# Kernel tuning notes

Measured on AMD Instinct MI355X. Metric: run time of the kernel, lower is better.

## Reference

```python
import jax, jax.numpy as jnp
import numpy as np

# geomloss SamplesLoss('sinkhorn', blur=0.5, scaling=0.9, reach=None) defaults: p=2, debias=True
P = 2
BLUR = 0.5
SCALING = 0.9


def _sqdist_half(a, b):
    # C(x,y) = |x-y|^2 / 2  (geomloss p=2 cost), shape [N, M]
    a2 = jnp.sum(a * a, axis=1)
    b2 = jnp.sum(b * b, axis=1)
    return 0.5 * (a2[:, None] + b2[None, :]) - a @ b.T


def _softmin(eps, C, h):
    # softmin_tensorized: -eps * logsumexp_j( h_j - C_ij / eps ),  h = log-weights + dual/eps
    return -eps * jax.nn.logsumexp(h[None, :] - C / eps, axis=1)


def _eps_schedule(x, y):
    # geomloss epsilon_schedule: anneal eps from diameter^p down to blur^p by scaling^p
    xn, yn = np.asarray(x), np.asarray(y)
    mins = np.minimum(xn.min(axis=0), yn.min(axis=0))
    maxs = np.maximum(xn.max(axis=0), yn.max(axis=0))
    diameter = float(np.linalg.norm(maxs - mins))
    eps_list = [diameter ** P]
    eps_list += [float(np.exp(e)) for e in
                 np.arange(P * np.log(diameter), P * np.log(BLUR), P * np.log(SCALING))]
    eps_list += [BLUR ** P]
    return eps_list


def _sinkhorn_divergence(x, y, eps_list):
    N, M = x.shape[0], y.shape[0]
    C_xy = _sqdist_half(x, y)
    C_yx = C_xy.T
    C_xx = _sqdist_half(x, x)
    C_yy = _sqdist_half(y, y)
    a_log = jnp.full((N,), -float(np.log(N)), dtype=x.dtype)  # uniform weights, log domain
    b_log = jnp.full((M,), -float(np.log(M)), dtype=x.dtype)

    sg = jax.lax.stop_gradient
    Cxy_d, Cyx_d = sg(C_xy), sg(C_yx)
    Cxx_d, Cyy_d = sg(C_xx), sg(C_yy)

    # init at largest eps (= diameter^p)
    eps0 = eps_list[0]
    f_ba = _softmin(eps0, Cxy_d, b_log)
    g_ab = _softmin(eps0, Cyx_d, a_log)
    f_aa = _softmin(eps0, Cxx_d, a_log)
    g_bb = _softmin(eps0, Cyy_d, b_log)

    # symmetric (averaged) Sinkhorn updates along the eps-scaling schedule (no grad, like geomloss)
    for eps in eps_list:
        ft_ba = _softmin(eps, Cxy_d, b_log + g_ab / eps)
        gt_ab = _softmin(eps, Cyx_d, a_log + f_ba / eps)
        ft_aa = _softmin(eps, Cxx_d, a_log + f_aa / eps)
        gt_bb = _softmin(eps, Cyy_d, b_log + g_bb / eps)
        f_ba, g_ab = 0.5 * (f_ba + ft_ba), 0.5 * (g_ab + gt_ab)
        f_aa, g_bb = 0.5 * (f_aa + ft_aa), 0.5 * (g_bb + gt_bb)

    # last extrapolation at eps = blur^p; gradient flows only through the cost matrices here
    eps = eps_list[-1]
    f_ba, g_ab = (_softmin(eps, C_xy, sg(b_log + g_ab / eps)),
                  _softmin(eps, C_yx, sg(a_log + f_ba / eps)))
    f_aa = _softmin(eps, C_xx, sg(a_log + f_aa / eps))
    g_bb = _softmin(eps, C_yy, sg(b_log + g_bb / eps))

    # debiased divergence: <alpha, f_ba - f_aa> + <beta, g_ab - g_bb> (uniform weights -> mean)
    return jnp.mean(f_ba - f_aa) + jnp.mean(g_ab - g_bb)


def setup_inputs() -> dict:
    key = jax.random.key(0)
    kx, ky = jax.random.split(key)
    x = jax.random.normal(kx, (4096, 32), dtype=jnp.float32)
    y = jax.random.normal(ky, (4096, 32), dtype=jnp.float32)
    return {"x": x, "y": y}


def reference(x, y):
    eps_list = _eps_schedule(x, y)  # data-dependent schedule computed eagerly (as geomloss does)
    return _sinkhorn_divergence(x, y, eps_list)
```

## Files before the change

### kernel.cpp

```cpp
#include <hip/hip_runtime.h>
#include <math.h>

#define NPTS 4096
#define DIM  32
#define MAXSLOTS 50
#define NTHREADS 256
#define ITHREADS 512
#define NELEM 131072

#define WS_N2X   0
#define WS_N2Y   4096
#define WS_PMIN  8192
#define WS_PMAX  10240
#define WS_EPS   12288
#define WS_MODE  12352
#define WS_DUAL  12416
#define DUALSZ   16384
#define WS_BF    45184

#define M_SKIP   0
#define M_INIT   1
#define M_AVG    2
#define M_ASSIGN 3

typedef short    short8 __attribute__((ext_vector_type(8)));
typedef _Float16 half8  __attribute__((ext_vector_type(8)));
typedef float    f32x4  __attribute__((ext_vector_type(4)));

__device__ __forceinline__ float exp2fast(float a){
#if __has_builtin(__builtin_amdgcn_exp2f)
    return __builtin_amdgcn_exp2f(a);
#else
    return exp2f(a);
#endif
}
__device__ __forceinline__ float log2fast(float a){
#if __has_builtin(__builtin_amdgcn_logf)
    return __builtin_amdgcn_logf(a);
#else
    return log2f(a);
#endif
}

__device__ __forceinline__ short8 pack8(const float* src){
    float4 v0 = ((const float4*)src)[0];
    float4 v1 = ((const float4*)src)[1];
    float vs[8] = {v0.x, v0.y, v0.z, v0.w, v1.x, v1.y, v1.z, v1.w};
    short hv[8];
#pragma unroll
    for (int i = 0; i < 8; i++) {
        union { _Float16 f; short s; } u;
        u.f = (_Float16)vs[i];
        hv[i] = u.s;
    }
    short8 r = {hv[0],hv[1],hv[2],hv[3],hv[4],hv[5],hv[6],hv[7]};
    return r;
}

__global__ void sink_setup(const float* __restrict__ x, const float* __restrict__ y,
                           float* __restrict__ ws, unsigned short* __restrict__ bf)
{
    __shared__ float2 mm[8][32];
    const int t = threadIdx.x;
    const int b = blockIdx.x;
    const int gtid = b * 256 + t;

    {
        int e = gtid * 8;
        *(short8*)((short*)bf + e)         = pack8(x + e);
        *(short8*)((short*)bf + NELEM + e) = pack8(y + e);
    }
    if (gtid < 2 * NPTS) {
        const float* src = (gtid < NPTS) ? (x + (size_t)gtid * DIM)
                                         : (y + (size_t)(gtid - NPTS) * DIM);
        const float4* s4 = (const float4*)src;
        float acc = 0.f;
#pragma unroll
        for (int q = 0; q < 8; q++) {
            float4 v = s4[q];
            acc += v.x*v.x + v.y*v.y + v.z*v.z + v.w*v.w;
        }
        ws[gtid] = 0.5f * acc;
    }
    {
        int d = t & 31, rg = t >> 5;
        float mn = 3.4e38f, mx = -3.4e38f;
#pragma unroll
        for (int k = 0; k < 16; k++) {
            int row = b * 128 + k * 8 + rg;
            const float* src = (row < NPTS) ? (x + (size_t)row * DIM)
                                            : (y + (size_t)(row - NPTS) * DIM);
            float v = src[d];
            mn = fminf(mn, v); mx = fmaxf(mx, v);
        }
        mm[rg][d] = make_float2(mn, mx);
    }
    __syncthreads();
    if (t < 32) {
        float2 a = mm[0][t];
#pragma unroll
        for (int g = 1; g < 8; g++) {
            float2 p = mm[g][t];
            a.x = fminf(a.x, p.x); a.y = fmaxf(a.y, p.y);
        }
        ws[WS_PMIN + b * 32 + t] = a.x;
        ws[WS_PMAX + b * 32 + t] = a.y;
    }
}

__global__ void sink_sched(float* __restrict__ ws)
{
    __shared__ float mins[32], maxs[32];
    int t = threadIdx.x;
    if (t < 32) {
        float mn = 3.4e38f, mx = -3.4e38f;
        for (int b = 0; b < 64; b++) {
            mn = fminf(mn, ws[WS_PMIN + b * 32 + t]);
            mx = fmaxf(mx, ws[WS_PMAX + b * 32 + t]);
        }
        mins[t] = mn; maxs[t] = mx;
    }
    __syncthreads();
    if (t == 0) {
        float dia2 = 0.f;
        for (int d = 0; d < 32; d++) {
            float df = maxs[d] - mins[d];
            dia2 += df * df;
        }
        float dia = sqrtf(dia2);
        float* eps = ws + WS_EPS;
        int*  mode = (int*)(ws + WS_MODE);
        double ld    = log((double)dia);
        double start = 2.0 * ld;
        double stop  = 2.0 * log(0.5);
        double step  = 2.0 * log(0.9);
        int K = (int)ceil((stop - start) / step);
        if (K < 0) K = 0;
        if (K > MAXSLOTS - 4) K = MAXSLOTS - 4;
        eps[0] = dia * dia; mode[0] = M_INIT;
        eps[1] = dia * dia; mode[1] = M_AVG;
        for (int k = 0; k < K; k++) {
            eps[2 + k] = (float)exp(start + step * (double)k);
            mode[2 + k] = M_AVG;
        }
        eps[2 + K] = 0.25f; mode[2 + K] = M_AVG;
        eps[3 + K] = 0.25f; mode[3 + K] = M_ASSIGN;
        for (int s = 4 + K; s < MAXSLOTS; s++) { eps[s] = 0.25f; mode[s] = M_SKIP; }
        mode[62] = K + 4;
    }
}

#define GLSE(T, R, G) \
    { float v0 = fmaf(ca##T[0][R], ie2, hpq[(G)*4 + 0]); \
      float v1 = fmaf(ca##T[1][R], ie2, hpq[(G)*4 + 1]); \
      float v2 = fmaf(ca##T[2][R], ie2, hpq[(G)*4 + 2]); \
      float v3 = fmaf(ca##T[3][R], ie2, hpq[(G)*4 + 3]); \
      float gm = fmaxf(fmaxf(v0, v1), v2); \
      float nm = fmaxf(fmaxf(gm, v3), ms##T[R]); \
      float er = exp2fast(ms##T[R] - nm); \
      float e0 = exp2fast(v0 - nm); \
      float e1 = exp2fast(v1 - nm); \
      float e2 = exp2fast(v2 - nm); \
      float e3 = exp2fast(v3 - nm); \
      ss##T[R] = fmaf(ss##T[R], er, (e0 + e1) + (e2 + e3)); \
      ms##T[R] = nm; }

__global__ __launch_bounds__(ITHREADS, 4) void sink_iter(float* __restrict__ ws, int slot)
{
    const int t = threadIdx.x;
    const int mode = ((const int*)(ws + WS_MODE))[slot];
    if (mode == M_SKIP) return;

    const float eps     = ws[WS_EPS + slot];
    const float inv_eps = 1.0f / eps;
    const float L2E     = 1.4426950408889634f;
    const float LN2     = 0.6931471805599453f;
    const float ie2     = inv_eps * L2E;
    const float hbase   = -8.317766166719343f;
    const float don     = (mode == M_INIT) ? 0.0f : 1.0f;

    const int bm   = blockIdx.x >> 7;
    const int tile = blockIdx.x & 127;
    const int S    = (blockIdx.x * 5) & 31;
    const int rowIsX = (bm == 0 || bm == 2);
    const int colIsX = (bm == 1 || bm == 2);

    const short* bf = (const short*)(ws + WS_BF);
    const short* rbase = bf + (rowIsX ? 0 : NELEM);
    const short* cbase = bf + (colIsX ? 0 : NELEM);
    const float* rn2 = ws + (rowIsX ? WS_N2X : WS_N2Y);
    const float* cn2 = ws + (colIsX ? WS_N2X : WS_N2Y);

    const float* bufold = ws + WS_DUAL + (slot & 1) * DUALSZ;
    float*       bufnew = ws + WS_DUAL + ((slot + 1) & 1) * DUALSZ;
    const int dualsel = (bm == 0) ? 1 : (bm == 1) ? 0 : bm;
    const float* dual   = bufold + dualsel * NPTS;
    const float* oldout = bufold + bm * NPTS;
    float*       out    = bufnew + bm * NPTS;

    __shared__ float2 parts[8][32];

    const int lane = t & 63;
    const int wv   = t >> 6;
    const int lr   = lane & 15;
    const int lk   = (lane >> 4) * 8;

    const int ar0 = tile * 32 + lr;
    const half8 a0 = *(const half8*)(rbase + ar0 * DIM + lk);
    const half8 a1 = *(const half8*)(rbase + (ar0 + 16) * DIM + lk);

    const int colbase = wv * 512;
    const short* cwb = cbase + (size_t)colbase * DIM;
    const int laneoff = lr * DIM + lk;

    float hpq[32];
#pragma unroll
    for (int p = 0; p < 32; p++) {
        const int j = colbase + ((p + S) & 31) * 16 + lr;
        hpq[p] = (hbase + fmaf(don, dual[j], -cn2[j]) * inv_eps) * L2E;
    }

    half8 bh[4];
#pragma unroll
    for (int p = 0; p < 4; p++) {
        const int w = (p + S) & 31;
        bh[p] = *(const half8*)(cwb + w * (16 * DIM) + laneoff);
    }

    float ms0[4] = {-INFINITY, -INFINITY, -INFINITY, -INFINITY};
    float ms1[4] = {-INFINITY, -INFINITY, -INFINITY, -INFINITY};
    float ss0[4] = {0.f, 0.f, 0.f, 0.f};
    float ss1[4] = {0.f, 0.f, 0.f, 0.f};
    f32x4 ca0[4], ca1[4];

#pragma unroll
    for (int g = 0; g < 8; g++) {
#pragma unroll
        for (int sl = 0; sl < 4; sl++) {
            const int ct = g * 4 + sl;
            const half8 hB = bh[sl];
            f32x4 u0 = {0.f, 0.f, 0.f, 0.f};
            f32x4 u1 = {0.f, 0.f, 0.f, 0.f};
            u0 = __builtin_amdgcn_mfma_f32_16x16x32_f16(a0, hB, u0, 0, 0, 0);
            u1 = __builtin_amdgcn_mfma_f32_16x16x32_f16(a1, hB, u1, 0, 0, 0);
            if (ct < 28) {
                const int w = ((ct + 4) + S) & 31;
                bh[sl] = *(const half8*)(cwb + w * (16 * DIM) + laneoff);
            }
            ca0[sl] = u0;
            ca1[sl] = u1;
        }
        GLSE(0, 0, g) GLSE(0, 1, g) GLSE(0, 2, g) GLSE(0, 3, g)
        GLSE(1, 0, g) GLSE(1, 1, g) GLSE(1, 2, g) GLSE(1, 3, g)
    }

#pragma unroll
    for (int wm = 1; wm <= 8; wm <<= 1) {
#pragma unroll
        for (int r = 0; r < 4; r++) {
            float om, os, nm;
            om = __shfl_xor(ms0[r], wm, 64); os = __shfl_xor(ss0[r], wm, 64);
            nm = fmaxf(ms0[r], om);
            ss0[r] = fmaf(ss0[r], exp2fast(ms0[r] - nm), os * exp2fast(om - nm));
            ms0[r] = nm;
            om = __shfl_xor(ms1[r], wm, 64); os = __shfl_xor(ss1[r], wm, 64);
            nm = fmaxf(ms1[r], om);
            ss1[r] = fmaf(ss1[r], exp2fast(ms1[r] - nm), os * exp2fast(om - nm));
            ms1[r] = nm;
        }
    }
    if (lr == 0) {
        const int g4 = (lane >> 4) * 4;
#pragma unroll
        for (int r = 0; r < 4; r++) {
            parts[wv][g4 + r]      = make_float2(ms0[r], ss0[r]);
            parts[wv][16 + g4 + r] = make_float2(ms1[r], ss1[r]);
        }
    }
    __syncthreads();
    if (t < 32) {
        float2 p = parts[0][t];
        float m = p.x, s = p.y;
#pragma unroll
        for (int w2 = 1; w2 < 8; w2++) {
            float2 q = parts[w2][t];
            float nm = fmaxf(m, q.x);
            s = fmaf(s, exp2fast(m - nm), q.y * exp2fast(q.x - nm));
            m = nm;
        }
        const float lse = LN2 * (m + log2fast(s));
        const int row = tile * 32 + t;
        const float ft = rn2[row] - eps * lse;
        out[row] = (mode == M_AVG) ? 0.5f * (oldout[row] + ft) : ft;
    }
}

__global__ void sink_reduce(const float* __restrict__ ws, float* __restrict__ outp)
{
    __shared__ float red[NTHREADS];
    const int niter = ((const int*)(ws + WS_MODE))[62];
    const float* b = ws + WS_DUAL + (niter & 1) * DUALSZ;
    int t = threadIdx.x;
    float acc = 0.f;
    for (int i = t; i < NPTS; i += NTHREADS)
        acc += (b[i] - b[2 * NPTS + i]) + (b[NPTS + i] - b[3 * NPTS + i]);
    red[t] = acc;
    __syncthreads();
    for (int s = NTHREADS / 2; s > 0; s >>= 1) {
        if (t < s) red[t] += red[t + s];
        __syncthreads();
    }
    if (t == 0) outp[0] = red[0] * (1.0f / (float)NPTS);
}

extern "C" void kernel_launch(void* const* d_in, const int* in_sizes, int n_in,
                              void* d_out, int out_size, void* d_ws, size_t ws_size,
                              hipStream_t stream)
{
    const float* x = (const float*)d_in[0];
    const float* y = (const float*)d_in[1];
    float* ws  = (float*)d_ws;
    float* out = (float*)d_out;

    hipLaunchKernelGGL(sink_setup, dim3(64), dim3(NTHREADS), 0, stream, x, y, ws,
                       (unsigned short*)(ws + WS_BF));
    hipLaunchKernelGGL(sink_sched, dim3(1),  dim3(NTHREADS), 0, stream, ws);
    for (int s = 0; s < MAXSLOTS; s++)
        hipLaunchKernelGGL(sink_iter, dim3(512), dim3(ITHREADS), 0, stream, ws, s);
    hipLaunchKernelGGL(sink_reduce, dim3(1), dim3(NTHREADS), 0, stream, ws, out);
}
```

Baseline: 912.7 us.

## Double block to 16 waves, stage dual potentials in LDS, shrink per-wave column span

Each block now runs 1024 threads (16 waves). Every wave covers 256 columns instead of 512, so each wave processes two column tiles per step instead of four. The per-column log-weight term is computed once per block into a shared-memory array rather than held in a 32-entry register array per thread, which cuts register pressure so more waves can be resident. The cost is an extra block-wide barrier, LDS reads inside the loop, and a 16-way final merge in place of an 8-way one. Fewer independent MFMAs per step may also hide latency less well.

After: 1.305 ms. 42.9% more time.

```diff
diff --git a/kernel.cpp b/kernel.cpp
--- a/kernel.cpp
+++ b/kernel.cpp
@@ -5,7 +5,7 @@
 #define DIM  32
 #define MAXSLOTS 50
 #define NTHREADS 256
-#define ITHREADS 512
+#define ITHREADS 1024
 #define NELEM 131072
 
 #define WS_N2X   0
@@ -150,22 +150,17 @@
     }
 }
 
-#define GLSE(T, R, G) \
-    { float v0 = fmaf(ca##T[0][R], ie2, hpq[(G)*4 + 0]); \
-      float v1 = fmaf(ca##T[1][R], ie2, hpq[(G)*4 + 1]); \
-      float v2 = fmaf(ca##T[2][R], ie2, hpq[(G)*4 + 2]); \
-      float v3 = fmaf(ca##T[3][R], ie2, hpq[(G)*4 + 3]); \
-      float gm = fmaxf(fmaxf(v0, v1), v2); \
-      float nm = fmaxf(fmaxf(gm, v3), ms##T[R]); \
+#define GLSE2(T, R) \
+    { float v0 = fmaf(ca##T[0][R], ie2, hpc0); \
+      float v1 = fmaf(ca##T[1][R], ie2, hpc1); \
+      float nm = fmaxf(fmaxf(v0, v1), ms##T[R]); \
       float er = exp2fast(ms##T[R] - nm); \
       float e0 = exp2fast(v0 - nm); \
       float e1 = exp2fast(v1 - nm); \
-      float e2 = exp2fast(v2 - nm); \
-      float e3 = exp2fast(v3 - nm); \
-      ss##T[R] = fmaf(ss##T[R], er, (e0 + e1) + (e2 + e3)); \
+      ss##T[R] = fmaf(ss##T[R], er, e0 + e1); \
       ms##T[R] = nm; }
 
-__global__ __launch_bounds__(ITHREADS, 4) void sink_iter(float* __restrict__ ws, int slot)
+__global__ __launch_bounds__(ITHREADS, 8) void sink_iter(float* __restrict__ ws, int slot)
 {
     const int t = threadIdx.x;
     const int mode = ((const int*)(ws + WS_MODE))[slot];
@@ -181,7 +176,7 @@
 
     const int bm   = blockIdx.x >> 7;
     const int tile = blockIdx.x & 127;
-    const int S    = (blockIdx.x * 5) & 31;
+    const int S    = (blockIdx.x * 5) & 15;
     const int rowIsX = (bm == 0 || bm == 2);
     const int colIsX = (bm == 1 || bm == 2);
 
@@ -198,7 +193,8 @@
     const float* oldout = bufold + bm * NPTS;
     float*       out    = bufnew + bm * NPTS;
 
-    __shared__ float2 parts[8][32];
+    __shared__ float  hps[NPTS];
+    __shared__ float2 parts[16][32];
 
     const int lane = t & 63;
     const int wv   = t >> 6;
@@ -209,49 +205,66 @@
     const half8 a0 = *(const half8*)(rbase + ar0 * DIM + lk);
     const half8 a1 = *(const half8*)(rbase + (ar0 + 16) * DIM + lk);
 
-    const int colbase = wv * 512;
+#pragma unroll
+    for (int q = 0; q < 4; q++) {
+        int j = t + q * ITHREADS;
+        hps[j] = (hbase + fmaf(don, dual[j], -cn2[j]) * inv_eps) * L2E;
+    }
+    __syncthreads();
+
+    const int colbase = wv * 256;
     const short* cwb = cbase + (size_t)colbase * DIM;
     const int laneoff = lr * DIM + lk;
-
-    float hpq[32];
-#pragma unroll
-    for (int p = 0; p < 32; p++) {
-        const int j = colbase + ((p + S) & 31) * 16 + lr;
-        hpq[p] = (hbase + fmaf(don, dual[j], -cn2[j]) * inv_eps) * L2E;
-    }
-
-    half8 bh[4];
-#pragma unroll
-    for (int p = 0; p < 4; p++) {
-        const int w = (p + S) & 31;
-        bh[p] = *(const half8*)(cwb + w * (16 * DIM) + laneoff);
+    const float* hpw = hps + colbase + lr;
+
+    half8 bh0, bh1;
+    float hpv0, hpv1;
+    {
+        const int w0 = S;
+        const int w1 = (1 + S) & 15;
+        bh0 = *(const half8*)(cwb + w0 * (16 * DIM) + laneoff);
+        bh1 = *(const half8*)(cwb + w1 * (16 * DIM) + laneoff);
+        hpv0 = hpw[w0 * 16];
+        hpv1 = hpw[w1 * 16];
     }
 
     float ms0[4] = {-INFINITY, -INFINITY, -INFINITY, -INFINITY};
     float ms1[4] = {-INFINITY, -INFINITY, -INFINITY, -INFINITY};
     float ss0[4] = {0.f, 0.f, 0.f, 0.f};
     float ss1[4] = {0.f, 0.f, 0.f, 0.f};
-    f32x4 ca0[4], ca1[4];
+    f32x4 ca0[2], ca1[2];
 
 #pragma unroll
     for (int g = 0; g < 8; g++) {
-#pragma unroll
-        for (int sl = 0; sl < 4; sl++) {
-            const int ct = g * 4 + sl;
-            const half8 hB = bh[sl];
+        float hpc0, hpc1;
+        {
             f32x4 u0 = {0.f, 0.f, 0.f, 0.f};
             f32x4 u1 = {0.f, 0.f, 0.f, 0.f};
-            u0 = __builtin_amdgcn_mfma_f32_16x16x32_f16(a0, hB, u0, 0, 0, 0);
-            u1 = __builtin_amdgcn_mfma_f32_16x16x32_f16(a1, hB, u1, 0, 0, 0);
-            if (ct < 28) {
-                const int w = ((ct + 4) + S) & 31;
-                bh[sl] = *(const half8*)(cwb + w * (16 * DIM) + laneoff);
+            u0 = __builtin_amdgcn_mfma_f32_16x16x32_f16(a0, bh0, u0, 0, 0, 0);
+            u1 = __builtin_amdgcn_mfma_f32_16x16x32_f16(a1, bh0, u1, 0, 0, 0);
+            hpc0 = hpv0;
+            if (g < 7) {
+                const int w = ((2 * g + 2) + S) & 15;
+                bh0  = *(const half8*)(cwb + w * (16 * DIM) + laneoff);
+                hpv0 = hpw[w * 16];
             }
-            ca0[sl] = u0;
-            ca1[sl] = u1;
-        }
-        GLSE(0, 0, g) GLSE(0, 1, g) GLSE(0, 2, g) GLSE(0, 3, g)
-        GLSE(1, 0, g) GLSE(1, 1, g) GLSE(1, 2, g) GLSE(1, 3, g)
+            ca0[0] = u0; ca1[0] = u1;
+        }
+        {
+            f32x4 u0 = {0.f, 0.f, 0.f, 0.f};
+            f32x4 u1 = {0.f, 0.f, 0.f, 0.f};
+            u0 = __builtin_amdgcn_mfma_f32_16x16x32_f16(a0, bh1, u0, 0, 0, 0);
+            u1 = __builtin_amdgcn_mfma_f32_16x16x32_f16(a1, bh1, u1, 0, 0, 0);
+            hpc1 = hpv1;
+            if (g < 7) {
+                const int w = ((2 * g + 3) + S) & 15;
+                bh1  = *(const half8*)(cwb + w * (16 * DIM) + laneoff);
+                hpv1 = hpw[w * 16];
+            }
+            ca0[1] = u0; ca1[1] = u1;
+        }
+        GLSE2(0, 0) GLSE2(0, 1) GLSE2(0, 2) GLSE2(0, 3)
+        GLSE2(1, 0) GLSE2(1, 1) GLSE2(1, 2) GLSE2(1, 3)
     }
 
 #pragma unroll
@@ -282,7 +295,7 @@
         float2 p = parts[0][t];
         float m = p.x, s = p.y;
 #pragma unroll
-        for (int w2 = 1; w2 < 8; w2++) {
+        for (int w2 = 1; w2 < 16; w2++) {
             float2 q = parts[w2][t];
             float nm = fmaxf(m, q.x);
             s = fmaf(s, exp2fast(m - nm), q.y * exp2fast(q.x - nm));
```

## Halve row tile to 16, precompute column potentials in LDS, double grid

Applied to the files above, without the earlier changes.

Each sink_iter block now handles 16 rows instead of 32, so the grid doubles to 1024 blocks and launch bounds target 8 blocks per CU. The per-column log-potential terms are computed once per block into shared memory rather than held as 32 registers per thread, and the B-fragment prefetch depth drops from 4 to 3. The aim is lower register pressure and higher occupancy to hide exp and MFMA latency. The cost is that every column fragment is now reused across half as many rows, doubling global traffic for B. It also adds a block-wide barrier and 16 KB of LDS per block, which can itself limit occupancy.

After: 963.4 us. 1.06x slower.

```diff
diff --git a/kernel.cpp b/kernel.cpp
--- a/kernel.cpp
+++ b/kernel.cpp
@@ -150,22 +150,22 @@
     }
 }
 
-#define GLSE(T, R, G) \
-    { float v0 = fmaf(ca##T[0][R], ie2, hpq[(G)*4 + 0]); \
-      float v1 = fmaf(ca##T[1][R], ie2, hpq[(G)*4 + 1]); \
-      float v2 = fmaf(ca##T[2][R], ie2, hpq[(G)*4 + 2]); \
-      float v3 = fmaf(ca##T[3][R], ie2, hpq[(G)*4 + 3]); \
+#define GLSE(R) \
+    { float v0 = fmaf(ca[0][R], ie2, hpr[0]); \
+      float v1 = fmaf(ca[1][R], ie2, hpr[1]); \
+      float v2 = fmaf(ca[2][R], ie2, hpr[2]); \
+      float v3 = fmaf(ca[3][R], ie2, hpr[3]); \
       float gm = fmaxf(fmaxf(v0, v1), v2); \
-      float nm = fmaxf(fmaxf(gm, v3), ms##T[R]); \
-      float er = exp2fast(ms##T[R] - nm); \
+      float nm = fmaxf(fmaxf(gm, v3), ms[R]); \
+      float er = exp2fast(ms[R] - nm); \
       float e0 = exp2fast(v0 - nm); \
       float e1 = exp2fast(v1 - nm); \
       float e2 = exp2fast(v2 - nm); \
       float e3 = exp2fast(v3 - nm); \
-      ss##T[R] = fmaf(ss##T[R], er, (e0 + e1) + (e2 + e3)); \
-      ms##T[R] = nm; }
-
-__global__ __launch_bounds__(ITHREADS, 4) void sink_iter(float* __restrict__ ws, int slot)
+      ss[R] = fmaf(ss[R], er, (e0 + e1) + (e2 + e3)); \
+      ms[R] = nm; }
+
+__global__ __launch_bounds__(ITHREADS, 8) void sink_iter(float* __restrict__ ws, int slot)
 {
     const int t = threadIdx.x;
     const int mode = ((const int*)(ws + WS_MODE))[slot];
@@ -179,8 +179,8 @@
     const float hbase   = -8.317766166719343f;
     const float don     = (mode == M_INIT) ? 0.0f : 1.0f;
 
-    const int bm   = blockIdx.x >> 7;
-    const int tile = blockIdx.x & 127;
+    const int bm   = blockIdx.x >> 8;
+    const int tile = blockIdx.x & 255;
     const int S    = (blockIdx.x * 5) & 31;
     const int rowIsX = (bm == 0 || bm == 2);
     const int colIsX = (bm == 1 || bm == 2);
@@ -198,87 +198,80 @@
     const float* oldout = bufold + bm * NPTS;
     float*       out    = bufnew + bm * NPTS;
 
-    __shared__ float2 parts[8][32];
+    __shared__ float  hps[NPTS];
+    __shared__ float2 parts[8][16];
 
     const int lane = t & 63;
     const int wv   = t >> 6;
     const int lr   = lane & 15;
     const int lk   = (lane >> 4) * 8;
 
-    const int ar0 = tile * 32 + lr;
-    const half8 a0 = *(const half8*)(rbase + ar0 * DIM + lk);
-    const half8 a1 = *(const half8*)(rbase + (ar0 + 16) * DIM + lk);
+    const int ar = tile * 16 + lr;
+    const half8 a0 = *(const half8*)(rbase + ar * DIM + lk);
+
+#pragma unroll
+    for (int q = 0; q < 8; q++) {
+        int j = t + q * ITHREADS;
+        hps[j] = (hbase + fmaf(don, dual[j], -cn2[j]) * inv_eps) * L2E;
+    }
+    __syncthreads();
 
     const int colbase = wv * 512;
     const short* cwb = cbase + (size_t)colbase * DIM;
     const int laneoff = lr * DIM + lk;
-
-    float hpq[32];
-#pragma unroll
-    for (int p = 0; p < 32; p++) {
-        const int j = colbase + ((p + S) & 31) * 16 + lr;
-        hpq[p] = (hbase + fmaf(don, dual[j], -cn2[j]) * inv_eps) * L2E;
-    }
-
-    half8 bh[4];
-#pragma unroll
-    for (int p = 0; p < 4; p++) {
+    const float* hpw = hps + colbase + lr;
+
+    half8 bh[3];
+    float hpv[3];
+#pragma unroll
+    for (int p = 0; p < 3; p++) {
         const int w = (p + S) & 31;
-        bh[p] = *(const half8*)(cwb + w * (16 * DIM) + laneoff);
-    }
-
-    float ms0[4] = {-INFINITY, -INFINITY, -INFINITY, -INFINITY};
-    float ms1[4] = {-INFINITY, -INFINITY, -INFINITY, -INFINITY};
-    float ss0[4] = {0.f, 0.f, 0.f, 0.f};
-    float ss1[4] = {0.f, 0.f, 0.f, 0.f};
-    f32x4 ca0[4], ca1[4];
-
-#pragma unroll
-    for (int g = 0; g < 8; g++) {
-#pragma unroll
-        for (int sl = 0; sl < 4; sl++) {
-            const int ct = g * 4 + sl;
-            const half8 hB = bh[sl];
-            f32x4 u0 = {0.f, 0.f, 0.f, 0.f};
-            f32x4 u1 = {0.f, 0.f, 0.f, 0.f};
-            u0 = __builtin_amdgcn_mfma_f32_16x16x32_f16(a0, hB, u0, 0, 0, 0);
-            u1 = __builtin_amdgcn_mfma_f32_16x16x32_f16(a1, hB, u1, 0, 0, 0);
-            if (ct < 28) {
-                const int w = ((ct + 4) + S) & 31;
-                bh[sl] = *(const half8*)(cwb + w * (16 * DIM) + laneoff);
-            }
-            ca0[sl] = u0;
-            ca1[sl] = u1;
-        }
-        GLSE(0, 0, g) GLSE(0, 1, g) GLSE(0, 2, g) GLSE(0, 3, g)
-        GLSE(1, 0, g) GLSE(1, 1, g) GLSE(1, 2, g) GLSE(1, 3, g)
+        bh[p]  = *(const half8*)(cwb + w * (16 * DIM) + laneoff);
+        hpv[p] = hpw[w * 16];
+    }
+
+    float ms[4] = {-INFINITY, -INFINITY, -INFINITY, -INFINITY};
+    float ss[4] = {0.f, 0.f, 0.f, 0.f};
+    f32x4 ca[4];
+    float hpr[4];
+
+#pragma unroll
+    for (int ct = 0; ct < 32; ct++) {
+        const int sl = ct % 3;
+        const half8 hB = bh[sl];
+        hpr[ct & 3] = hpv[sl];
+        f32x4 u = {0.f, 0.f, 0.f, 0.f};
+        u = __builtin_amdgcn_mfma_f32_16x16x32_f16(a0, hB, u, 0, 0, 0);
+        if (ct < 29) {
+            const int w = ((ct + 3) + S) & 31;
+            bh[sl]  = *(const half8*)(cwb + w * (16 * DIM) + laneoff);
+            hpv[sl] = hpw[w * 16];
+        }
+        ca[ct & 3] = u;
+        if ((ct & 3) == 3) {
+            GLSE(0) GLSE(1) GLSE(2) GLSE(3)
+        }
     }
 
 #pragma unroll
     for (int wm = 1; wm <= 8; wm <<= 1) {
 #pragma unroll
         for (int r = 0; r < 4; r++) {
-            float om, os, nm;
-            om = __shfl_xor(ms0[r], wm, 64); os = __shfl_xor(ss0[r], wm, 64);
-            nm = fmaxf(ms0[r], om);
-            ss0[r] = fmaf(ss0[r], exp2fast(ms0[r] - nm), os * exp2fast(om - nm));
-            ms0[r] = nm;
-            om = __shfl_xor(ms1[r], wm, 64); os = __shfl_xor(ss1[r], wm, 64);
-            nm = fmaxf(ms1[r], om);
-            ss1[r] = fmaf(ss1[r], exp2fast(ms1[r] - nm), os * exp2fast(om - nm));
-            ms1[r] = nm;
+            float om = __shfl_xor(ms[r], wm, 64);
+            float os = __shfl_xor(ss[r], wm, 64);
+            float nm = fmaxf(ms[r], om);
+            ss[r] = fmaf(ss[r], exp2fast(ms[r] - nm), os * exp2fast(om - nm));
+            ms[r] = nm;
         }
     }
     if (lr == 0) {
         const int g4 = (lane >> 4) * 4;
 #pragma unroll
-        for (int r = 0; r < 4; r++) {
-            parts[wv][g4 + r]      = make_float2(ms0[r], ss0[r]);
-            parts[wv][16 + g4 + r] = make_float2(ms1[r], ss1[r]);
-        }
-    }
-    __syncthreads();
-    if (t < 32) {
+        for (int r = 0; r < 4; r++)
+            parts[wv][g4 + r] = make_float2(ms[r], ss[r]);
+    }
+    __syncthreads();
+    if (t < 16) {
         float2 p = parts[0][t];
         float m = p.x, s = p.y;
 #pragma unroll
@@ -289,7 +282,7 @@
             m = nm;
         }
         const float lse = LN2 * (m + log2fast(s));
-        const int row = tile * 32 + t;
+        const int row = tile * 16 + t;
         const float ft = rn2[row] - eps * lse;
         out[row] = (mode == M_AVG) ? 0.5f * (oldout[row] + ft) : ft;
     }
@@ -326,6 +319,6 @@
                        (unsigned short*)(ws + WS_BF));
     hipLaunchKernelGGL(sink_sched, dim3(1),  dim3(NTHREADS), 0, stream, ws);
     for (int s = 0; s < MAXSLOTS; s++)
-        hipLaunchKernelGGL(sink_iter, dim3(512), dim3(ITHREADS), 0, stream, ws, s);
+        hipLaunchKernelGGL(sink_iter, dim3(1024), dim3(ITHREADS), 0, stream, ws, s);
     hipLaunchKernelGGL(sink_reduce, dim3(1), dim3(NTHREADS), 0, stream, ws, out);
 }
```

## Stage dual potentials in shared memory and deepen column prefetch to six tiles

Applied to the files above, without the earlier changes.

The block now computes the per-column log-potential vector once into a 16 KB shared array, instead of each thread precomputing 32 values into registers from global memory. The values are then read from shared memory alongside the B-fragment prefetch. The prefetch ring grows from 4 to 6 column tiles so more global loads are in flight while the MFMA/logsumexp loop runs. The goal is to cut redundant global loads and register pressure and to hide more load latency. In exchange it adds a __syncthreads, shared-memory traffic and extra LDS use per block, which may lower occupancy.

After: 882.9 us. 1.03x faster.

```diff
diff --git a/kernel.cpp b/kernel.cpp
--- a/kernel.cpp
+++ b/kernel.cpp
@@ -150,11 +150,11 @@
     }
 }
 
-#define GLSE(T, R, G) \
-    { float v0 = fmaf(ca##T[0][R], ie2, hpq[(G)*4 + 0]); \
-      float v1 = fmaf(ca##T[1][R], ie2, hpq[(G)*4 + 1]); \
-      float v2 = fmaf(ca##T[2][R], ie2, hpq[(G)*4 + 2]); \
-      float v3 = fmaf(ca##T[3][R], ie2, hpq[(G)*4 + 3]); \
+#define GLSE(T, R) \
+    { float v0 = fmaf(ca##T[0][R], ie2, hpr[0]); \
+      float v1 = fmaf(ca##T[1][R], ie2, hpr[1]); \
+      float v2 = fmaf(ca##T[2][R], ie2, hpr[2]); \
+      float v3 = fmaf(ca##T[3][R], ie2, hpr[3]); \
       float gm = fmaxf(fmaxf(v0, v1), v2); \
       float nm = fmaxf(fmaxf(gm, v3), ms##T[R]); \
       float er = exp2fast(ms##T[R] - nm); \
@@ -198,6 +198,7 @@
     const float* oldout = bufold + bm * NPTS;
     float*       out    = bufnew + bm * NPTS;
 
+    __shared__ float  hps[NPTS];
     __shared__ float2 parts[8][32];
 
     const int lane = t & 63;
@@ -209,49 +210,55 @@
     const half8 a0 = *(const half8*)(rbase + ar0 * DIM + lk);
     const half8 a1 = *(const half8*)(rbase + (ar0 + 16) * DIM + lk);
 
+#pragma unroll
+    for (int q = 0; q < 8; q++) {
+        int j = t + q * ITHREADS;
+        hps[j] = (hbase + fmaf(don, dual[j], -cn2[j]) * inv_eps) * L2E;
+    }
+    __syncthreads();
+
     const int colbase = wv * 512;
     const short* cwb = cbase + (size_t)colbase * DIM;
     const int laneoff = lr * DIM + lk;
-
-    float hpq[32];
-#pragma unroll
-    for (int p = 0; p < 32; p++) {
-        const int j = colbase + ((p + S) & 31) * 16 + lr;
-        hpq[p] = (hbase + fmaf(don, dual[j], -cn2[j]) * inv_eps) * L2E;
-    }
-
-    half8 bh[4];
-#pragma unroll
-    for (int p = 0; p < 4; p++) {
+    const float* hpw = hps + colbase + lr;
+
+    half8 bh[6];
+    float hpv[6];
+#pragma unroll
+    for (int p = 0; p < 6; p++) {
         const int w = (p + S) & 31;
-        bh[p] = *(const half8*)(cwb + w * (16 * DIM) + laneoff);
+        bh[p]  = *(const half8*)(cwb + w * (16 * DIM) + laneoff);
+        hpv[p] = hpw[w * 16];
     }
 
     float ms0[4] = {-INFINITY, -INFINITY, -INFINITY, -INFINITY};
     float ms1[4] = {-INFINITY, -INFINITY, -INFINITY, -INFINITY};
     float ss0[4] = {0.f, 0.f, 0.f, 0.f};
     float ss1[4] = {0.f, 0.f, 0.f, 0.f};
+
     f32x4 ca0[4], ca1[4];
-
-#pragma unroll
-    for (int g = 0; g < 8; g++) {
-#pragma unroll
-        for (int sl = 0; sl < 4; sl++) {
-            const int ct = g * 4 + sl;
-            const half8 hB = bh[sl];
-            f32x4 u0 = {0.f, 0.f, 0.f, 0.f};
-            f32x4 u1 = {0.f, 0.f, 0.f, 0.f};
-            u0 = __builtin_amdgcn_mfma_f32_16x16x32_f16(a0, hB, u0, 0, 0, 0);
-            u1 = __builtin_amdgcn_mfma_f32_16x16x32_f16(a1, hB, u1, 0, 0, 0);
-            if (ct < 28) {
-                const int w = ((ct + 4) + S) & 31;
-                bh[sl] = *(const half8*)(cwb + w * (16 * DIM) + laneoff);
-            }
-            ca0[sl] = u0;
-            ca1[sl] = u1;
-        }
-        GLSE(0, 0, g) GLSE(0, 1, g) GLSE(0, 2, g) GLSE(0, 3, g)
-        GLSE(1, 0, g) GLSE(1, 1, g) GLSE(1, 2, g) GLSE(1, 3, g)
+    float hpr[4];
+
+#pragma unroll
+    for (int ct = 0; ct < 32; ct++) {
+        const int sl = ct % 6;
+        const half8 hB = bh[sl];
+        hpr[ct & 3] = hpv[sl];
+        f32x4 u0 = {0.f, 0.f, 0.f, 0.f};
+        f32x4 u1 = {0.f, 0.f, 0.f, 0.f};
+        u0 = __builtin_amdgcn_mfma_f32_16x16x32_f16(a0, hB, u0, 0, 0, 0);
+        u1 = __builtin_amdgcn_mfma_f32_16x16x32_f16(a1, hB, u1, 0, 0, 0);
+        if (ct < 26) {
+            const int w = ((ct + 6) + S) & 31;
+            bh[sl]  = *(const half8*)(cwb + w * (16 * DIM) + laneoff);
+            hpv[sl] = hpw[w * 16];
+        }
+        ca0[ct & 3] = u0;
+        ca1[ct & 3] = u1;
+        if ((ct & 3) == 3) {
+            GLSE(0, 0) GLSE(0, 1) GLSE(0, 2) GLSE(0, 3)
+            GLSE(1, 0) GLSE(1, 1) GLSE(1, 2) GLSE(1, 3)
+        }
     }
 
 #pragma unroll
```
